# Optimization experiments

Hardware: AMD Instinct MI355X
Metric: run time of the kernel (lower is better)

The kernel has to match this reference:

```python
import jax, jax.numpy as jnp
import numpy as np

B, T, D, H = 2, 2048, 512, 8
HD = D // H
EPS = 1e-5


def setup_inputs() -> dict:
    key = jax.random.key(0)
    ks = jax.random.split(key, 8)
    s = 1.0 / np.sqrt(D)
    return {
        "x": jax.random.normal(ks[0], (B, T, D), dtype=jnp.float32),
        "Wq": jax.random.uniform(ks[1], (D, D), jnp.float32, -s, s),
        "bq": jnp.zeros((D,), jnp.float32),
        "Wk": jax.random.uniform(ks[2], (D, D), jnp.float32, -s, s),
        "bk": jnp.zeros((D,), jnp.float32),
        "Wv": jax.random.uniform(ks[3], (D, D), jnp.float32, -s, s),
        "bv": jnp.zeros((D,), jnp.float32),
        "gn_w": jnp.ones((D,), jnp.float32),
        "gn_b": jnp.zeros((D,), jnp.float32),
        "gamma": jnp.float32(0.9),
    }


def reference(x, Wq, bq, Wk, bk, Wv, bv, gn_w, gn_b, gamma):
    Bx, Tx, Dx = x.shape
    # projections (torch Linear: x @ W.T + b), split heads -> [B,H,T,hd]
    def proj(W, b):
        return (x @ W.T + b).reshape(Bx, Tx, H, HD).transpose(0, 2, 1, 3)
    Q, K, V = proj(Wq, bq), proj(Wk, bk), proj(Wv, bv)
    # retention scores with causal exponential decay mask
    attn = jnp.einsum("bhqd,bhkd->bhqk", Q, K)  # [B,H,T,T]
    idx = jnp.arange(Tx)
    diff = idx[:, None] - idx[None, :]
    # clamp negative exponents before pow to avoid inf (masked out anyway)
    decay = jnp.where(diff >= 0,
                      jnp.power(gamma, jnp.maximum(diff, 0).astype(jnp.float32)),
                      0.0)
    attn = attn * decay[None, None]
    out = jnp.einsum("bhqk,bhkd->bhqd", attn, V)  # [B,H,T,hd]
    out = out.transpose(0, 2, 1, 3)  # [B,T,H,hd]
    # GroupNorm over channels grouped by head; normalized over (T, hd) per (b, h)
    mean = out.mean(axis=(1, 3), keepdims=True)
    var = out.var(axis=(1, 3), keepdims=True)
    out = (out - mean) / jnp.sqrt(var + EPS)
    out = out.reshape(Bx, Tx, Dx) * gn_w + gn_b
    return out
```

## Files before the change

kernel.cpp:

```cpp
#include <hip/hip_runtime.h>
#include <math.h>

#define B_ 2
#define T_ 2048
#define D_ 512
#define H_ 8
#define HD_ 64
#define NG_ (B_*H_)
#define EPS_ 1e-5f

typedef __attribute__((ext_vector_type(8)))  short  short8;
typedef __attribute__((ext_vector_type(16))) float  floatx16;

__device__ inline floatx16 zero16() {
    floatx16 z;
#pragma unroll
    for (int i = 0; i < 16; i++) z[i] = 0.f;
    return z;
}

__device__ inline unsigned pack2bf(float a, float b) {
    unsigned ua = __float_as_uint(a), ub = __float_as_uint(b);
    ua = (ua + 0x7fffu + ((ua >> 16) & 1u)) >> 16;
    ub = (ub + 0x7fffu + ((ub >> 16) & 1u)) >> 16;
    return ua | (ub << 16);
}
__device__ inline short bf1(float a) {
    unsigned ua = __float_as_uint(a);
    return (short)((ua + 0x7fffu + ((ua >> 16) & 1u)) >> 16);
}

__global__ __launch_bounds__(256) void convert_w(
    const float* __restrict__ Wq, const float* __restrict__ Wk, const float* __restrict__ Wv,
    short* __restrict__ Wb, float* __restrict__ stats)
{
    if (blockIdx.x == 0 && threadIdx.x < 32) stats[threadIdx.x] = 0.f;
    const int WN = 512 * 512;
    size_t e = ((size_t)blockIdx.x * 256 + threadIdx.x) * 8;
    const float* src;
    if (e < WN)               src = Wq + e;
    else if (e < 2u * WN)     src = Wk + (e - WN);
    else                      src = Wv + (e - 2 * WN);
    float4 a = *(const float4*)src;
    float4 b = *(const float4*)(src + 4);
    uint4 o;
    o.x = pack2bf(a.x, a.y); o.y = pack2bf(a.z, a.w);
    o.z = pack2bf(b.x, b.y); o.w = pack2bf(b.z, b.w);
    *(uint4*)&Wb[e] = o;
}

__global__ __launch_bounds__(256, 3) void proj_mfma(
    const float* __restrict__ x, const short* __restrict__ Wb,
    const float* __restrict__ bq, const float* __restrict__ bk, const float* __restrict__ bv,
    short* __restrict__ Qo, short* __restrict__ Ko, short* __restrict__ Vto)
{
    __shared__ short Xs[2][64 * 64];
    __shared__ short Ws2[2][128 * 64];

    const int tid = threadIdx.x;
    const int w = tid >> 6, lane = tid & 63;
    const int hi = lane >> 5, ln = lane & 31;
    const int mt0 = blockIdx.x * 64;
    const int nt0 = blockIdx.y * 128;
    const int z = blockIdx.z;
    const bool isV = (z == 2);
    const float* bias = (z == 0) ? bq : (z == 1) ? bk : bv;
    const short* Wz = Wb + (size_t)z * 512 * 512;

    const int srow = tid >> 3;
    const int scol = (((tid & 7) ^ ((tid >> 3) & 7)) * 8);
    const int mh = w & 1, nh = w >> 1;

    floatx16 acc[2] = {zero16(), zero16()};
    float4 xr[2][2];

    auto gload_x = [&](int k0) {
#pragma unroll
        for (int i = 0; i < 2; i++) {
            const float* p = x + (size_t)(mt0 + srow + i * 32) * 512 + k0 + scol;
            xr[i][0] = *(const float4*)p;
            xr[i][1] = *(const float4*)(p + 4);
        }
    };
    auto spill_x = [&](int b) {
#pragma unroll
        for (int i = 0; i < 2; i++) {
            uint4 o;
            o.x = pack2bf(xr[i][0].x, xr[i][0].y);
            o.y = pack2bf(xr[i][0].z, xr[i][0].w);
            o.z = pack2bf(xr[i][1].x, xr[i][1].y);
            o.w = pack2bf(xr[i][1].z, xr[i][1].w);
            *(uint4*)&Xs[b][(srow + i * 32) * 64 + (tid & 7) * 8] = o;
        }
    };
    auto glds_w = [&](int b, int k0) {
#pragma unroll
        for (int i = 0; i < 4; i++) {
            const short* gw = Wz + (size_t)(nt0 + srow + i * 32) * 512 + k0 + scol;
            short* lw = &Ws2[b][(srow + i * 32) * 64 + (tid & 7) * 8];
            __builtin_amdgcn_global_load_lds(
                (const __attribute__((address_space(1))) unsigned*)gw,
                (__attribute__((address_space(3))) unsigned*)lw, 16, 0, 0);
        }
    };

    gload_x(0);
    glds_w(0, 0);
    int buf = 0;
    for (int k0 = 0; k0 < 512; k0 += 64, buf ^= 1) {
        spill_x(buf);
        __syncthreads();
        if (k0 + 64 < 512) { gload_x(k0 + 64); glds_w(buf ^ 1, k0 + 64); }
#pragma unroll
        for (int kk = 0; kk < 4; kk++) {
            const int gx = ((2 * kk + hi) ^ (ln & 7)) * 8;
            short8 xf = *(const short8*)(&Xs[buf][(mh * 32 + ln) * 64 + gx]);
            short8 wf[2];
#pragma unroll
            for (int s = 0; s < 2; s++)
                wf[s] = *(const short8*)(&Ws2[buf][(nh * 64 + s * 32 + ln) * 64 + gx]);
#pragma unroll
            for (int b = 0; b < 2; b++)
                acc[b] = isV
                    ? __builtin_amdgcn_mfma_f32_32x32x16_bf16(wf[b], xf, acc[b], 0, 0, 0)
                    : __builtin_amdgcn_mfma_f32_32x32x16_bf16(xf, wf[b], acc[b], 0, 0, 0);
        }
    }

    const int head = blockIdx.y * 2 + nh;

    if (!isV) {
        short* dst = (z == 0) ? Qo : Ko;
        float bias_v[2];
#pragma unroll
        for (int b = 0; b < 2; b++) bias_v[b] = bias[nt0 + nh * 64 + b * 32 + ln];
#pragma unroll
        for (int r = 0; r < 16; r++) {
            int m = mt0 + mh * 32 + (r & 3) + 8 * (r >> 2) + 4 * hi;
            int batch = m >> 11, t = m & (T_ - 1);
            size_t rowb = ((size_t)(batch * H_ + head) * T_ + t) * HD_;
#pragma unroll
            for (int b = 0; b < 2; b++)
                dst[rowb + b * 32 + ln] = bf1(acc[b][r] + bias_v[b]);
        }
    } else {
        const int m = mt0 + mh * 32 + ln;
        const int batch = m >> 11, t = m & (T_ - 1);
#pragma unroll
        for (int b = 0; b < 2; b++) {
#pragma unroll
            for (int r = 0; r < 16; r++) {
                int chan = nt0 + nh * 64 + b * 32 + (r & 3) + 8 * (r >> 2) + 4 * hi;
                int d = chan & (HD_ - 1);
                Vto[((size_t)(batch * H_ + head) * HD_ + d) * T_ + t] = bf1(acc[b][r] + bias[chan]);
            }
        }
    }
}

__global__ __launch_bounds__(256, 2) void retention_kernel(
    const short* __restrict__ Q, const short* __restrict__ K, const short* __restrict__ Vt,
    const float* __restrict__ gamma_p,
    float* __restrict__ out,
    float* __restrict__ stats)
{
    __shared__ float red[3][32 * 64];

    const int tid  = threadIdx.x;
    const int ks   = tid >> 6, lane = tid & 63;
    const int hi   = lane >> 5, ln = lane & 31;
    const int g    = blockIdx.x, qtt = blockIdx.y;
    const int q0   = qtt * 32;
    const int qt   = qtt >> 1;

    const float gamma = gamma_p[0];
    const float lg = logf(gamma);
    int kt0 = 0;
    if (lg < -1e-6f) {
        int maxd = (int)(-13.0f / lg) + 64;
        kt0 = qt - (maxd >> 6);
        if (kt0 < 0) kt0 = 0;
    }

    const short* Qbase = Q + ((size_t)g * T_ + q0 + ln) * HD_;
    short8 qf[4];
#pragma unroll
    for (int c = 0; c < 4; c++) qf[c] = *(const short8*)(Qbase + 16 * c + 8 * hi);

    const float Alane = __expf(lg * (float)(ln - 4 * hi));
    const float G32   = __expf(-lg * 32.0f);
    float Ea[4], Eb[4];
#pragma unroll
    for (int j = 0; j < 4; j++) { Ea[j] = __expf(-lg * (float)j); Eb[j] = __expf(-lg * (float)(8 * j)); }
    const int qrel = (qtt & 1) * 32 + ln;

    floatx16 oacc[2] = {zero16(), zero16()};

    int kt = kt0 + ((ks - kt0) & 3);
    short8 kf[2][4];
    if (kt <= qt) {
        const short* Kbase = K + ((size_t)g * T_ + kt * 64) * HD_;
#pragma unroll
        for (int kh = 0; kh < 2; kh++)
#pragma unroll
            for (int c = 0; c < 4; c++)
                kf[kh][c] = *(const short8*)(Kbase + (size_t)(kh * 32 + ln) * HD_ + 16 * c + 8 * hi);
    }

    for (; kt <= qt; kt += 4) {
        const int k0 = kt * 64;

        floatx16 st[2];
#pragma unroll
        for (int kh = 0; kh < 2; kh++) {
            floatx16 acc = zero16();
#pragma unroll
            for (int c = 0; c < 4; c++)
                acc = __builtin_amdgcn_mfma_f32_32x32x16_bf16(kf[kh][c], qf[c], acc, 0, 0, 0);
            st[kh] = acc;
        }

        short8 vf[4][2];
#pragma unroll
        for (int c = 0; c < 4; c++)
#pragma unroll
            for (int dh = 0; dh < 2; dh++)
                vf[c][dh] = *(const short8*)(Vt + ((size_t)g * HD_ + dh * 32 + ln) * T_ + k0 + 16 * c + 8 * hi);

        const int ktn = kt + 4;
        if (ktn <= qt) {
            const short* Kn = K + ((size_t)g * T_ + ktn * 64) * HD_;
#pragma unroll
            for (int kh = 0; kh < 2; kh++)
#pragma unroll
                for (int c = 0; c < 4; c++)
                    kf[kh][c] = *(const short8*)(Kn + (size_t)(kh * 32 + ln) * HD_ + 16 * c + 8 * hi);
        }

        const float Ckt = __expf(lg * (float)(q0 - k0));
        const float base0 = Alane * Ckt;
        const bool diag = (kt == qt);
#pragma unroll
        for (int kh = 0; kh < 2; kh++) {
            float bb = base0 * (kh ? G32 : 1.0f);
#pragma unroll
            for (int r = 0; r < 16; r++) {
                float v = st[kh][r] * (bb * Ea[r & 3] * Eb[r >> 2]);
                if (diag) {
                    int kloc = kh * 32 + (r & 3) + 8 * (r >> 2) + 4 * hi;
                    if (qrel < kloc) v = 0.f;
                }
                st[kh][r] = v;
            }
        }

#pragma unroll
        for (int c = 0; c < 4; c++) {
            const int kh = c >> 1, rb = 8 * (c & 1);
            unsigned p0 = pack2bf(st[kh][rb+0], st[kh][rb+1]);
            unsigned p1 = pack2bf(st[kh][rb+2], st[kh][rb+3]);
            unsigned p2 = pack2bf(st[kh][rb+4], st[kh][rb+5]);
            unsigned p3 = pack2bf(st[kh][rb+6], st[kh][rb+7]);
            unsigned t0s = (unsigned)__shfl_xor((int)(hi ? p0 : p2), 32, 64);
            unsigned t1s = (unsigned)__shfl_xor((int)(hi ? p1 : p3), 32, 64);
            uint4 aw;
            aw.x = hi ? t0s : p0;  aw.y = hi ? t1s : p1;
            aw.z = hi ? p2  : t0s; aw.w = hi ? p3  : t1s;
            short8 afr = *reinterpret_cast<short8*>(&aw);
#pragma unroll
            for (int dh = 0; dh < 2; dh++)
                oacc[dh] = __builtin_amdgcn_mfma_f32_32x32x16_bf16(afr, vf[c][dh], oacc[dh], 0, 0, 0);
        }
    }

    if (ks) {
        float* rp = &red[ks - 1][0];
#pragma unroll
        for (int dh = 0; dh < 2; dh++)
#pragma unroll
            for (int r = 0; r < 16; r++) {
                int qloc = (r & 3) + 8 * (r >> 2) + 4 * hi;
                rp[qloc * 64 + dh * 32 + ln] = oacc[dh][r];
            }
    }
    __syncthreads();
    if (ks == 0) {
        const int b = g >> 3, h = g & 7;
        float sm = 0.f, sq = 0.f;
#pragma unroll
        for (int dh = 0; dh < 2; dh++)
#pragma unroll
            for (int r = 0; r < 16; r++) {
                int qloc = (r & 3) + 8 * (r >> 2) + 4 * hi;
                int col = qloc * 64 + dh * 32 + ln;
                float v = oacc[dh][r] + red[0][col] + red[1][col] + red[2][col];
                int q = q0 + qloc;
                out[((size_t)(b * T_ + q)) * D_ + h * 64 + dh * 32 + ln] = v;
                sm += v; sq += v * v;
            }
        for (int off = 32; off > 0; off >>= 1) {
            sm += __shfl_down(sm, off);
            sq += __shfl_down(sq, off);
        }
        if (lane == 0) {
            atomicAdd(&stats[g], sm);
            atomicAdd(&stats[NG_ + g], sq);
        }
    }
}

__global__ __launch_bounds__(256) void norm_kernel(
    float* __restrict__ out, const float* __restrict__ stats,
    const float* __restrict__ gn_w, const float* __restrict__ gn_b)
{
    int idx4 = blockIdx.x * 256 + threadIdx.x;
    if (idx4 >= (B_ * T_ * D_) / 4) return;
    int base = idx4 * 4;
    int c0 = base & (D_ - 1);
    int b = base >> 20;
    int g = b * H_ + (c0 >> 6);
    const float invN = 1.f / (float)(T_ * HD_);
    float mean = stats[g] * invN;
    float var  = stats[NG_ + g] * invN - mean * mean;
    float inv  = rsqrtf(var + EPS_);
    float4 v = *(float4*)&out[base];
    float4 wv = *(const float4*)&gn_w[c0];
    float4 bv = *(const float4*)&gn_b[c0];
    v.x = (v.x - mean) * inv * wv.x + bv.x;
    v.y = (v.y - mean) * inv * wv.y + bv.y;
    v.z = (v.z - mean) * inv * wv.z + bv.z;
    v.w = (v.w - mean) * inv * wv.w + bv.w;
    *(float4*)&out[base] = v;
}

extern "C" void kernel_launch(void* const* d_in, const int* in_sizes, int n_in,
                              void* d_out, int out_size, void* d_ws, size_t ws_size,
                              hipStream_t stream)
{
    const float* x    = (const float*)d_in[0];
    const float* Wq   = (const float*)d_in[1];
    const float* bq   = (const float*)d_in[2];
    const float* Wk   = (const float*)d_in[3];
    const float* bk   = (const float*)d_in[4];
    const float* Wv   = (const float*)d_in[5];
    const float* bv   = (const float*)d_in[6];
    const float* gn_w = (const float*)d_in[7];
    const float* gn_b = (const float*)d_in[8];
    const float* gam  = (const float*)d_in[9];
    float* out = (float*)d_out;

    const size_t per = (size_t)B_ * H_ * T_ * HD_;
    float* stats = (float*)d_ws;
    short* Qw  = (short*)((char*)d_ws + 256);
    short* Kw  = Qw + per;
    short* Vtw = Kw + per;
    short* Wb  = Vtw + per;

    convert_w<<<384, 256, 0, stream>>>(Wq, Wk, Wv, Wb, stats);
    proj_mfma<<<dim3(64, 4, 3), 256, 0, stream>>>(x, Wb, bq, bk, bv, Qw, Kw, Vtw);
    retention_kernel<<<dim3(16, 64), 256, 0, stream>>>(Qw, Kw, Vtw, gam, out, stats);
    norm_kernel<<<2048, 256, 0, stream>>>(out, stats, gn_w, gn_b);
}
```

Measured before the change: 118.8 us.

## Fuse weight conversion into projection and GroupNorm into retention tail

Removes the separate weight-conversion kernel: the projection now loads fp32 weights into registers and converts them to bf16 while writing to LDS, and adds a second barrier per k-step. The standalone norm kernel is removed as well. Each retention block bumps a per-group counter, and the last block for a group applies the normalization to that group's output slice. This drops two launches and one full pass over the output, at the cost of serializing the normalization into 16 blocks and adding register pressure in the projection.

```diff
diff --git a/kernel.cpp b/kernel.cpp
--- a/kernel.cpp
+++ b/kernel.cpp
@@ -29,35 +29,29 @@
     unsigned ua = __float_as_uint(a);
     return (short)((ua + 0x7fffu + ((ua >> 16) & 1u)) >> 16);
 }
-
-__global__ __launch_bounds__(256) void convert_w(
-    const float* __restrict__ Wq, const float* __restrict__ Wk, const float* __restrict__ Wv,
-    short* __restrict__ Wb, float* __restrict__ stats)
-{
-    if (blockIdx.x == 0 && threadIdx.x < 32) stats[threadIdx.x] = 0.f;
-    const int WN = 512 * 512;
-    size_t e = ((size_t)blockIdx.x * 256 + threadIdx.x) * 8;
-    const float* src;
-    if (e < WN)               src = Wq + e;
-    else if (e < 2u * WN)     src = Wk + (e - WN);
-    else                      src = Wv + (e - 2 * WN);
-    float4 a = *(const float4*)src;
-    float4 b = *(const float4*)(src + 4);
+__device__ inline uint4 pack8bf(const float4& a, const float4& b) {
     uint4 o;
     o.x = pack2bf(a.x, a.y); o.y = pack2bf(a.z, a.w);
     o.z = pack2bf(b.x, b.y); o.w = pack2bf(b.z, b.w);
-    *(uint4*)&Wb[e] = o;
+    return o;
 }
 
 __global__ __launch_bounds__(256, 3) void proj_mfma(
-    const float* __restrict__ x, const short* __restrict__ Wb,
+    const float* __restrict__ x,
+    const float* __restrict__ Wq, const float* __restrict__ Wk, const float* __restrict__ Wv,
     const float* __restrict__ bq, const float* __restrict__ bk, const float* __restrict__ bv,
-    short* __restrict__ Qo, short* __restrict__ Ko, short* __restrict__ Vto)
+    short* __restrict__ Qo, short* __restrict__ Ko, short* __restrict__ Vto,
+    float* __restrict__ stats, int* __restrict__ counter)
 {
     __shared__ short Xs[2][64 * 64];
     __shared__ short Ws2[2][128 * 64];
 
     const int tid = threadIdx.x;
+    if (blockIdx.x == 0 && blockIdx.y == 0 && blockIdx.z == 0) {
+        if (tid < 32) stats[tid] = 0.f;
+        if (tid < 16) counter[tid] = 0;
+    }
+
     const int w = tid >> 6, lane = tid & 63;
     const int hi = lane >> 5, ln = lane & 31;
     const int mt0 = blockIdx.x * 64;
@@ -65,7 +59,7 @@
     const int z = blockIdx.z;
     const bool isV = (z == 2);
     const float* bias = (z == 0) ? bq : (z == 1) ? bk : bv;
-    const short* Wz = Wb + (size_t)z * 512 * 512;
+    const float* Wz = (z == 0) ? Wq : (z == 1) ? Wk : Wv;
 
     const int srow = tid >> 3;
     const int scol = (((tid & 7) ^ ((tid >> 3) & 7)) * 8);
@@ -73,44 +67,38 @@
 
     floatx16 acc[2] = {zero16(), zero16()};
     float4 xr[2][2];
-
-    auto gload_x = [&](int k0) {
+    float4 wr[4][2];
+
+    auto gload = [&](int k0) {
 #pragma unroll
         for (int i = 0; i < 2; i++) {
             const float* p = x + (size_t)(mt0 + srow + i * 32) * 512 + k0 + scol;
             xr[i][0] = *(const float4*)p;
             xr[i][1] = *(const float4*)(p + 4);
         }
+#pragma unroll
+        for (int i = 0; i < 4; i++) {
+            const float* p = Wz + (size_t)(nt0 + srow + i * 32) * 512 + k0 + scol;
+            wr[i][0] = *(const float4*)p;
+            wr[i][1] = *(const float4*)(p + 4);
+        }
     };
-    auto spill_x = [&](int b) {
-#pragma unroll
-        for (int i = 0; i < 2; i++) {
-            uint4 o;
-            o.x = pack2bf(xr[i][0].x, xr[i][0].y);
-            o.y = pack2bf(xr[i][0].z, xr[i][0].w);
-            o.z = pack2bf(xr[i][1].x, xr[i][1].y);
-            o.w = pack2bf(xr[i][1].z, xr[i][1].w);
-            *(uint4*)&Xs[b][(srow + i * 32) * 64 + (tid & 7) * 8] = o;
-        }
+    auto spill = [&](int b) {
+        const int slot = (tid & 7) * 8;
+#pragma unroll
+        for (int i = 0; i < 2; i++)
+            *(uint4*)&Xs[b][(srow + i * 32) * 64 + slot] = pack8bf(xr[i][0], xr[i][1]);
+#pragma unroll
+        for (int i = 0; i < 4; i++)
+            *(uint4*)&Ws2[b][(srow + i * 32) * 64 + slot] = pack8bf(wr[i][0], wr[i][1]);
     };
-    auto glds_w = [&](int b, int k0) {
-#pragma unroll
-        for (int i = 0; i < 4; i++) {
-            const short* gw = Wz + (size_t)(nt0 + srow + i * 32) * 512 + k0 + scol;
-            short* lw = &Ws2[b][(srow + i * 32) * 64 + (tid & 7) * 8];
-            __builtin_amdgcn_global_load_lds(
-                (const __attribute__((address_space(1))) unsigned*)gw,
-                (__attribute__((address_space(3))) unsigned*)lw, 16, 0, 0);
-        }
-    };
-
-    gload_x(0);
-    glds_w(0, 0);
+
+    gload(0);
     int buf = 0;
     for (int k0 = 0; k0 < 512; k0 += 64, buf ^= 1) {
-        spill_x(buf);
+        spill(buf);
         __syncthreads();
-        if (k0 + 64 < 512) { gload_x(k0 + 64); glds_w(buf ^ 1, k0 + 64); }
+        if (k0 + 64 < 512) gload(k0 + 64);
 #pragma unroll
         for (int kk = 0; kk < 4; kk++) {
             const int gx = ((2 * kk + hi) ^ (ln & 7)) * 8;
@@ -125,6 +113,7 @@
                     ? __builtin_amdgcn_mfma_f32_32x32x16_bf16(wf[b], xf, acc[b], 0, 0, 0)
                     : __builtin_amdgcn_mfma_f32_32x32x16_bf16(xf, wf[b], acc[b], 0, 0, 0);
         }
+        __syncthreads();
     }
 
     const int head = blockIdx.y * 2 + nh;
@@ -161,10 +150,14 @@
 __global__ __launch_bounds__(256, 2) void retention_kernel(
     const short* __restrict__ Q, const short* __restrict__ K, const short* __restrict__ Vt,
     const float* __restrict__ gamma_p,
+    const float* __restrict__ gn_w, const float* __restrict__ gn_b,
     float* __restrict__ out,
-    float* __restrict__ stats)
+    float* __restrict__ stats,
+    int* __restrict__ counter)
 {
     __shared__ float red[3][32 * 64];
+    __shared__ int   finFlag;
+    __shared__ float msh[2];
 
     const int tid  = threadIdx.x;
     const int ks   = tid >> 6, lane = tid & 63;
@@ -284,8 +277,8 @@
             }
     }
     __syncthreads();
+    const int b = g >> 3, h = g & 7;
     if (ks == 0) {
-        const int b = g >> 3, h = g & 7;
         float sm = 0.f, sq = 0.f;
 #pragma unroll
         for (int dh = 0; dh < 2; dh++)
@@ -307,30 +300,39 @@
             atomicAdd(&stats[NG_ + g], sq);
         }
     }
-}
-
-__global__ __launch_bounds__(256) void norm_kernel(
-    float* __restrict__ out, const float* __restrict__ stats,
-    const float* __restrict__ gn_w, const float* __restrict__ gn_b)
-{
-    int idx4 = blockIdx.x * 256 + threadIdx.x;
-    if (idx4 >= (B_ * T_ * D_) / 4) return;
-    int base = idx4 * 4;
-    int c0 = base & (D_ - 1);
-    int b = base >> 20;
-    int g = b * H_ + (c0 >> 6);
-    const float invN = 1.f / (float)(T_ * HD_);
-    float mean = stats[g] * invN;
-    float var  = stats[NG_ + g] * invN - mean * mean;
-    float inv  = rsqrtf(var + EPS_);
-    float4 v = *(float4*)&out[base];
-    float4 wv = *(const float4*)&gn_w[c0];
-    float4 bv = *(const float4*)&gn_b[c0];
-    v.x = (v.x - mean) * inv * wv.x + bv.x;
-    v.y = (v.y - mean) * inv * wv.y + bv.y;
-    v.z = (v.z - mean) * inv * wv.z + bv.z;
-    v.w = (v.w - mean) * inv * wv.w + bv.w;
-    *(float4*)&out[base] = v;
+
+    if (tid == 0) {
+        __threadfence();
+        int old = __hip_atomic_fetch_add(&counter[g], 1, __ATOMIC_ACQ_REL,
+                                         __HIP_MEMORY_SCOPE_AGENT);
+        finFlag = (old == NG_ * 4 - 1 - (NG_ * 4 - 64 - 1) - 1);
+        finFlag = (old == 63);
+        if (finFlag) {
+            __threadfence();
+            float s1 = __hip_atomic_load(&stats[g], __ATOMIC_RELAXED, __HIP_MEMORY_SCOPE_AGENT);
+            float s2 = __hip_atomic_load(&stats[NG_ + g], __ATOMIC_RELAXED, __HIP_MEMORY_SCOPE_AGENT);
+            const float invN = 1.f / (float)(T_ * HD_);
+            float mean = s1 * invN;
+            float var  = s2 * invN - mean * mean;
+            msh[0] = mean;
+            msh[1] = rsqrtf(var + EPS_);
+        }
+    }
+    __syncthreads();
+    if (finFlag) {
+        const float mean = msh[0], inv = msh[1];
+        float4 wv = *(const float4*)&gn_w[h * 64 + (tid & 15) * 4];
+        float4 bv = *(const float4*)&gn_b[h * 64 + (tid & 15) * 4];
+        for (int row = tid >> 4; row < T_; row += 16) {
+            float* p = &out[((size_t)(b * T_ + row)) * D_ + h * 64 + (tid & 15) * 4];
+            float4 v = *(float4*)p;
+            v.x = (v.x - mean) * inv * wv.x + bv.x;
+            v.y = (v.y - mean) * inv * wv.y + bv.y;
+            v.z = (v.z - mean) * inv * wv.z + bv.z;
+            v.w = (v.w - mean) * inv * wv.w + bv.w;
+            *(float4*)p = v;
+        }
+    }
 }
 
 extern "C" void kernel_launch(void* const* d_in, const int* in_sizes, int n_in,
@@ -350,14 +352,14 @@
     float* out = (float*)d_out;
 
     const size_t per = (size_t)B_ * H_ * T_ * HD_;
-    float* stats = (float*)d_ws;
+    float* stats   = (float*)d_ws;
+    int*   counter = (int*)((char*)d_ws + 128);
     short* Qw  = (short*)((char*)d_ws + 256);
     short* Kw  = Qw + per;
     short* Vtw = Kw + per;
-    short* Wb  = Vtw + per;
-
-    convert_w<<<384, 256, 0, stream>>>(Wq, Wk, Wv, Wb, stats);
-    proj_mfma<<<dim3(64, 4, 3), 256, 0, stream>>>(x, Wb, bq, bk, bv, Qw, Kw, Vtw);
-    retention_kernel<<<dim3(16, 64), 256, 0, stream>>>(Qw, Kw, Vtw, gam, out, stats);
-    norm_kernel<<<2048, 256, 0, stream>>>(out, stats, gn_w, gn_b);
-}
+
+    proj_mfma<<<dim3(64, 4, 3), 256, 0, stream>>>(x, Wq, Wk, Wv, bq, bk, bv,
+                                                  Qw, Kw, Vtw, stats, counter);
+    retention_kernel<<<dim3(16, 64), 256, 0, stream>>>(Qw, Kw, Vtw, gam,
+                                                       gn_w, gn_b, out, stats, counter);
+}
```

Result: slower. 197.3 us (+66.1%).
